# Performance work log

Measured on AMD Instinct MI355X. Metric: run time of the kernel, lower is better.

The kernel has to match this reference:

```python
import jax, jax.numpy as jnp
import numpy as np

EMBED_DIM = 1024
NUM_HEADS = 16
HEAD_DIM = EMBED_DIM // NUM_HEADS


def setup_inputs() -> dict:
    key = jax.random.key(0)
    k1, k2, k3 = jax.random.split(key, 3)
    B, S = 2, 2048
    x = jax.random.normal(k1, (B, S, EMBED_DIM), dtype=jnp.float32)
    # Xavier-uniform-style init for dense kernels
    lim_qkv = float(np.sqrt(6.0 / (EMBED_DIM + 3 * EMBED_DIM)))
    w_qkv = jax.random.uniform(k2, (EMBED_DIM, 3 * EMBED_DIM), jnp.float32, -lim_qkv, lim_qkv)
    b_qkv = jnp.zeros((3 * EMBED_DIM,), jnp.float32)
    lim_out = float(np.sqrt(6.0 / (EMBED_DIM + EMBED_DIM)))
    w_out = jax.random.uniform(k3, (EMBED_DIM, EMBED_DIM), jnp.float32, -lim_out, lim_out)
    b_out = jnp.zeros((EMBED_DIM,), jnp.float32)
    return {"x": x, "w_qkv": w_qkv, "b_qkv": b_qkv, "w_out": w_out, "b_out": b_out}


def reference(x, w_qkv, b_qkv, w_out, b_out):
    B, S, E = x.shape
    qkv = x @ w_qkv + b_qkv                       # [B, S, 3E]
    qkv = qkv.reshape(B, S, NUM_HEADS, 3 * HEAD_DIM)
    qkv = qkv.transpose(0, 2, 1, 3)               # [B, H, S, 3*dh]
    q, k, v = jnp.split(qkv, 3, axis=-1)          # each [B, H, S, dh]
    scale = 1.0 / jnp.sqrt(jnp.asarray(HEAD_DIM, x.dtype))
    logits = jnp.einsum('bhqd,bhkd->bhqk', q, k) * scale  # [B, H, S, S]
    attn = jax.nn.softmax(logits, axis=-1)
    vals = jnp.einsum('bhqk,bhkd->bhqd', attn, v)  # [B, H, S, dh]
    vals = vals.transpose(0, 2, 1, 3).reshape(B, S, E)
    return vals @ w_out + b_out
```

## Files before the change

kernel.cpp:

```cpp
#include <hip/hip_runtime.h>
#include <cstdint>

typedef unsigned short u16;
typedef unsigned int u32;
typedef __attribute__((ext_vector_type(8))) short bf16x8;
typedef __attribute__((ext_vector_type(4))) float f32x4;

#if __has_builtin(__builtin_amdgcn_exp2f)
#define EXP2(x) __builtin_amdgcn_exp2f(x)
#else
#define EXP2(x) exp2f(x)
#endif

__device__ __forceinline__ u16 f2bf(float f) {
  unsigned u = __float_as_uint(f);
  u += 0x7fffu + ((u >> 16) & 1u);
  return (u16)(u >> 16);
}
__device__ __forceinline__ u32 pk_bf16(float lo, float hi) {
#if __has_builtin(__builtin_amdgcn_cvt_pk_bf16_f32)
  auto r = __builtin_amdgcn_cvt_pk_bf16_f32(lo, hi);
  return __builtin_bit_cast(u32, r);
#else
  u32 a = __float_as_uint(lo), b = __float_as_uint(hi);
  a += 0x7fffu + ((a >> 16) & 1u);
  b += 0x7fffu + ((b >> 16) & 1u);
  return (a >> 16) | (b & 0xffff0000u);
#endif
}

__device__ __forceinline__ void async_load16(const void* g, void* l) {
  typedef const __attribute__((address_space(1))) void* gp_t;
  typedef __attribute__((address_space(3))) void* lp_t;
  __builtin_amdgcn_global_load_lds((gp_t)(uintptr_t)g, (lp_t)(uintptr_t)l, 16, 0, 0);
}

__global__ __launch_bounds__(256) void cvt_f32_bf16(
    const float* __restrict__ src, u16* __restrict__ dst)
{
  const size_t i = ((size_t)blockIdx.x * 256 + threadIdx.x) * 8;
  const float4 a = *(const float4*)(src + i);
  const float4 b = *(const float4*)(src + i + 4);
  union { u16 u[8]; bf16x8 v; } p;
  p.u[0] = f2bf(a.x); p.u[1] = f2bf(a.y); p.u[2] = f2bf(a.z); p.u[3] = f2bf(a.w);
  p.u[4] = f2bf(b.x); p.u[5] = f2bf(b.y); p.u[6] = f2bf(b.z); p.u[7] = f2bf(b.w);
  *(bf16x8*)(dst + i) = p.v;
}

__global__ __launch_bounds__(256) void transpose_cvt2(
    const float* __restrict__ wqkv, u16* __restrict__ dqkv,
    const float* __restrict__ wout, u16* __restrict__ dout)
{
  __shared__ u16 tile[64][65];
  const int t = threadIdx.x;
  const int r = t >> 2, c0 = (t & 3) * 16;
  const bool isOut = blockIdx.x >= 48;
  const float* src = isOut ? wout : wqkv;
  u16* dst = isOut ? dout : dqkv;
  const int cols = isOut ? 1024 : 3072;
  const int rows = 1024;
  const int tc = (isOut ? (blockIdx.x - 48) : blockIdx.x) * 64;
  const int tr = blockIdx.y * 64;
  const float* sp = src + (size_t)(tr + r) * cols + tc + c0;
#pragma unroll
  for (int i = 0; i < 16; i += 4) {
    const float4 v = *(const float4*)(sp + i);
    tile[r][c0 + i + 0] = f2bf(v.x);
    tile[r][c0 + i + 1] = f2bf(v.y);
    tile[r][c0 + i + 2] = f2bf(v.z);
    tile[r][c0 + i + 3] = f2bf(v.w);
  }
  __syncthreads();
  u16* dp = dst + (size_t)(tc + r) * rows + tr + c0;
#pragma unroll
  for (int i = 0; i < 16; ++i) dp[i] = tile[c0 + i][r];
}

__global__ __launch_bounds__(256) void transpose_v(
    const u16* __restrict__ src, u16* __restrict__ dst)
{
  __shared__ u16 tile[64][72];
  const int t = threadIdx.x;
  const int r = t >> 2, c0 = (t & 3) * 16;
  const int bh = blockIdx.y, s0 = blockIdx.x * 64;
  const u16* sp = src + ((size_t)bh * 2048 + s0 + r) * 64 + c0;
  union { u16 u[8]; bf16x8 v; } a, b;
  a.v = *(const bf16x8*)sp;
  b.v = *(const bf16x8*)(sp + 8);
#pragma unroll
  for (int i = 0; i < 8; ++i) tile[r][c0 + i] = a.u[i];
#pragma unroll
  for (int i = 0; i < 8; ++i) tile[r][c0 + 8 + i] = b.u[i];
  __syncthreads();
  union { u16 u[8]; bf16x8 v; } x, y;
#pragma unroll
  for (int i = 0; i < 8; ++i) x.u[i] = tile[c0 + i][r];
#pragma unroll
  for (int i = 0; i < 8; ++i) y.u[i] = tile[c0 + 8 + i][r];
  u16* dp = dst + ((size_t)bh * 64 + r) * 2048 + s0 + c0;
  *(bf16x8*)dp = x.v;
  *(bf16x8*)(dp + 8) = y.v;
}

__global__ __launch_bounds__(256) void gemm_qkv(
    const u16* __restrict__ A, const u16* __restrict__ Bt, const float* __restrict__ bias,
    u16* __restrict__ Qp, u16* __restrict__ Kp, u16* __restrict__ Vp, int Kd)
{
  __shared__ __align__(16) u16 As[128 * 32];
  __shared__ __align__(16) u16 Bs[128 * 32];
  const int t = threadIdx.x;
  const int lane = t & 63, wave = t >> 6;
  const int quad = lane >> 4, m16 = lane & 15;
  const int mb = blockIdx.y * 128, nb = blockIdx.x * 128;
  const int wr = (wave & 1) * 64, wc = (wave >> 1) * 64;

  const int srow = t >> 2;
  const int scol = (t & 3) * 8;
  const u16* Ag0 = A + (size_t)(mb + srow) * Kd + scol;
  const u16* Ag1 = Ag0 + (size_t)64 * Kd;
  const u16* Bg0 = Bt + (size_t)(nb + srow) * Kd + scol;
  const u16* Bg1 = Bg0 + (size_t)64 * Kd;
  u16* AsD = As + t * 8;
  u16* BsD = Bs + t * 8;

  f32x4 acc[4][4] = {};

  for (int k0 = 0; k0 < Kd; k0 += 32) {
    __syncthreads();
    async_load16(Ag0 + k0, AsD);
    async_load16(Ag1 + k0, AsD + 2048);
    async_load16(Bg0 + k0, BsD);
    async_load16(Bg1 + k0, BsD + 2048);
    __syncthreads();
    bf16x8 af[4], bfr[4];
#pragma unroll
    for (int i = 0; i < 4; ++i)
      af[i] = *(const bf16x8*)(As + (wr + i * 16 + m16) * 32 + quad * 8);
#pragma unroll
    for (int i = 0; i < 4; ++i)
      bfr[i] = *(const bf16x8*)(Bs + (wc + i * 16 + m16) * 32 + quad * 8);
#pragma unroll
    for (int i = 0; i < 4; ++i)
#pragma unroll
      for (int j = 0; j < 4; ++j)
        acc[i][j] = __builtin_amdgcn_mfma_f32_16x16x32_bf16(af[i], bfr[j], acc[i][j], 0, 0, 0);
  }

#pragma unroll
  for (int j = 0; j < 4; ++j) {
    const int base = nb + wc + j * 16;
    const float bv = bias[base + m16];
    const int seg = base >> 6;
    const int h = seg / 3;
    const int which = seg - h * 3;
    const int d = (base & 63) + m16;
    const float qs = (which == 0) ? 0.18033688011112042f : 1.0f;
#pragma unroll
    for (int i = 0; i < 4; ++i)
#pragma unroll
      for (int r = 0; r < 4; ++r) {
        const int row = mb + wr + i * 16 + quad * 4 + r;
        const int b = row >> 11, sI = row & 2047;
        const u16 v = f2bf((acc[i][j][r] + bv) * qs);
        const size_t idx = (((size_t)((b << 4) | h)) * 2048 + sI) * 64 + d;
        if (which == 0)      Qp[idx] = v;
        else if (which == 1) Kp[idx] = v;
        else                 Vp[idx] = v;
      }
  }
}

__global__ __launch_bounds__(256) void gemm_out(
    const u16* __restrict__ A, const u16* __restrict__ Bt, const float* __restrict__ bias,
    float* __restrict__ Outp)
{
  const int Kd = 1024;
  __shared__ __align__(16) u16 As[64 * 32];
  __shared__ __align__(16) u16 Bs[128 * 32];
  const int t = threadIdx.x;
  const int lane = t & 63, wave = t >> 6;
  const int quad = lane >> 4, m16 = lane & 15;
  const int mb = blockIdx.y * 64, nb = blockIdx.x * 128;
  const int wr = (wave & 1) * 32, wc = (wave >> 1) * 64;

  const int srow = t >> 2;
  const int scol = (t & 3) * 8;
  const u16* Ag0 = A + (size_t)(mb + srow) * Kd + scol;
  const u16* Bg0 = Bt + (size_t)(nb + srow) * Kd + scol;
  const u16* Bg1 = Bg0 + (size_t)64 * Kd;
  u16* AsD = As + t * 8;
  u16* BsD = Bs + t * 8;

  f32x4 acc[2][4] = {};

  for (int k0 = 0; k0 < Kd; k0 += 32) {
    __syncthreads();
    async_load16(Ag0 + k0, AsD);
    async_load16(Bg0 + k0, BsD);
    async_load16(Bg1 + k0, BsD + 2048);
    __syncthreads();
    bf16x8 af[2], bfr[4];
#pragma unroll
    for (int i = 0; i < 2; ++i)
      af[i] = *(const bf16x8*)(As + (wr + i * 16 + m16) * 32 + quad * 8);
#pragma unroll
    for (int j = 0; j < 4; ++j)
      bfr[j] = *(const bf16x8*)(Bs + (wc + j * 16 + m16) * 32 + quad * 8);
#pragma unroll
    for (int i = 0; i < 2; ++i)
#pragma unroll
      for (int j = 0; j < 4; ++j)
        acc[i][j] = __builtin_amdgcn_mfma_f32_16x16x32_bf16(af[i], bfr[j], acc[i][j], 0, 0, 0);
  }

#pragma unroll
  for (int j = 0; j < 4; ++j) {
    const int col = nb + wc + j * 16 + m16;
    const float bv = bias[col];
#pragma unroll
    for (int i = 0; i < 2; ++i)
#pragma unroll
      for (int r = 0; r < 4; ++r) {
        const int row = mb + wr + i * 16 + quad * 4 + r;
        Outp[(size_t)row * 1024 + col] = acc[i][j][r] + bv;
      }
  }
}

__global__ __launch_bounds__(256) void flash_attn(
    const u16* __restrict__ Q, const u16* __restrict__ K, const u16* __restrict__ Vt,
    u16* __restrict__ O)
{
  const int S = 2048;
  __shared__ __align__(16) u16 Kl[2][64 * 64];
  __shared__ __align__(16) u16 Vl[2][64 * 64];
  __shared__ __align__(16) u32 Pl[4][2][16 * 32];
  const int t = threadIdx.x;
  const int lane = t & 63, w = t >> 6;
  const int quad = lane >> 4, m16 = lane & 15;

  const int f = blockIdx.x;
  const int wi = f >> 3;
  const int bh = (f & 7) + 8 * (wi & 3);
  const int q0 = (wi >> 2) * 128;

  const u16* Qb = Q + (size_t)bh * S * 64;
  const u16* Kb = K + (size_t)bh * S * 64;
  const u16* Vb = Vt + (size_t)bh * 64 * S;

  bf16x8 qf[2][2];
#pragma unroll
  for (int g = 0; g < 2; ++g)
#pragma unroll
    for (int ks = 0; ks < 2; ++ks)
      qf[g][ks] = *(const bf16x8*)(Qb + (size_t)(q0 + w * 32 + g * 16 + m16) * 64 + ks * 32 + quad * 8);

  const u16* Kg[2]; const u16* Vg[2]; int soff[2];
#pragma unroll
  for (int l = 0; l < 2; ++l) {
    const int idx = l * 256 + t;
    const int row = idx >> 3, slot = idx & 7;
    const int sg = slot ^ (row & 7);
    Kg[l] = Kb + row * 64 + sg * 8;
    Vg[l] = Vb + (size_t)row * S + sg * 8;
    soff[l] = idx * 8;
  }

  f32x4 ot[2][4] = {};
  f32x4 lr4[2] = {{0.f,0.f,0.f,0.f},{0.f,0.f,0.f,0.f}};
  u32* const Pw0 = &Pl[w][0][0];
  u32* const Pw1 = &Pl[w][1][0];

#define PREFETCH(kvp, B)                                                     \
  do {                                                                       \
    _Pragma("unroll")                                                        \
    for (int l = 0; l < 2; ++l) async_load16(Kg[l] + (kvp) * 64, &Kl[B][soff[l]]); \
    _Pragma("unroll")                                                        \
    for (int l = 0; l < 2; ++l) async_load16(Vg[l] + (kvp), &Vl[B][soff[l]]);      \
  } while (0)

#define STEP(B)                                                              \
  do {                                                                       \
    f32x4 st[2][4] = {};                                                     \
    _Pragma("unroll")                                                        \
    for (int nt = 0; nt < 4; ++nt) {                                         \
      const int j = nt * 16 + m16;                                           \
      const u16* rowp = &Kl[B][j * 64];                                      \
      const bf16x8 kb0 = *(const bf16x8*)(rowp + ((quad ^ (j & 7)) * 8));    \
      const bf16x8 kb1 = *(const bf16x8*)(rowp + (((4 + quad) ^ (j & 7)) * 8)); \
      st[0][nt] = __builtin_amdgcn_mfma_f32_16x16x32_bf16(kb0, qf[0][0], st[0][nt], 0, 0, 0); \
      st[1][nt] = __builtin_amdgcn_mfma_f32_16x16x32_bf16(kb0, qf[1][0], st[1][nt], 0, 0, 0); \
      st[0][nt] = __builtin_amdgcn_mfma_f32_16x16x32_bf16(kb1, qf[0][1], st[0][nt], 0, 0, 0); \
      st[1][nt] = __builtin_amdgcn_mfma_f32_16x16x32_bf16(kb1, qf[1][1], st[1][nt], 0, 0, 0); \
    }                                                                        \
    _Pragma("unroll")                                                        \
    for (int g = 0; g < 2; ++g) {                                            \
      u32* const Pw = g ? Pw1 : Pw0;                                         \
      _Pragma("unroll")                                                      \
      for (int nt = 0; nt < 4; ++nt) {                                       \
        f32x4 p;                                                             \
        _Pragma("unroll")                                                    \
        for (int r = 0; r < 4; ++r) p[r] = EXP2(st[g][nt][r]);               \
        lr4[g] += p;                                                         \
        const u32 lo = pk_bf16(p[0], p[1]);                                  \
        const u32 hi = pk_bf16(p[2], p[3]);                                  \
        const int gp = (2 * nt + (quad >> 1)) ^ (m16 & 7);                   \
        u32* dst = Pw + m16 * 32 + gp * 4 + (quad & 1) * 2;                  \
        *(uint2*)dst = make_uint2(lo, hi);                                   \
      }                                                                      \
    }                                                                        \
    _Pragma("unroll")                                                        \
    for (int ks = 0; ks < 2; ++ks) {                                         \
      const int pg = (ks * 4 + quad) ^ (m16 & 7);                            \
      const bf16x8 pb0 = *(const bf16x8*)(Pw0 + m16 * 32 + pg * 4);          \
      const bf16x8 pb1 = *(const bf16x8*)(Pw1 + m16 * 32 + pg * 4);          \
      _Pragma("unroll")                                                      \
      for (int dt = 0; dt < 4; ++dt) {                                       \
        const int d = dt * 16 + m16;                                         \
        const bf16x8 va = *(const bf16x8*)(&Vl[B][d * 64] + (((ks * 4 + quad) ^ (d & 7)) * 8)); \
        ot[0][dt] = __builtin_amdgcn_mfma_f32_16x16x32_bf16(va, pb0, ot[0][dt], 0, 0, 0); \
        ot[1][dt] = __builtin_amdgcn_mfma_f32_16x16x32_bf16(va, pb1, ot[1][dt], 0, 0, 0); \
      }                                                                      \
    }                                                                        \
  } while (0)

  PREFETCH(0, 0);
  __syncthreads();

  for (int kv0 = 0; kv0 < S; kv0 += 128) {
    PREFETCH(kv0 + 64, 1);
    STEP(0);
    __syncthreads();
    if (kv0 + 128 < S) PREFETCH(kv0 + 128, 0);
    STEP(1);
    __syncthreads();
  }
#undef PREFETCH
#undef STEP

  const int b = bh >> 4, h = bh & 15;
#pragma unroll
  for (int g = 0; g < 2; ++g) {
    float l = lr4[g][0] + lr4[g][1] + lr4[g][2] + lr4[g][3];
    l += __shfl_xor(l, 16, 64);
    l += __shfl_xor(l, 32, 64);
    const float inv = 1.0f / l;
    const int q = q0 + w * 32 + g * 16 + m16;
    u16* base = O + ((size_t)b * 2048 + q) * 1024 + h * 64;
#pragma unroll
    for (int dt = 0; dt < 4; ++dt) {
      const u32 lo = pk_bf16(ot[g][dt][0] * inv, ot[g][dt][1] * inv);
      const u32 hi = pk_bf16(ot[g][dt][2] * inv, ot[g][dt][3] * inv);
      *(uint2*)(base + dt * 16 + quad * 4) = make_uint2(lo, hi);
    }
  }
}

extern "C" void kernel_launch(void* const* d_in, const int* in_sizes, int n_in,
                              void* d_out, int out_size, void* d_ws, size_t ws_size,
                              hipStream_t stream)
{
  const float* x     = (const float*)d_in[0];
  const float* w_qkv = (const float*)d_in[1];
  const float* b_qkv = (const float*)d_in[2];
  const float* w_out = (const float*)d_in[3];
  const float* b_out = (const float*)d_in[4];
  float* out = (float*)d_out;

  u16* ws     = (u16*)d_ws;
  u16* xb     = ws;
  u16* WtQKV  = xb + 4194304;
  u16* WtOut  = WtQKV + 3145728;
  u16* Qm     = WtOut + 1048576;
  u16* Km     = Qm + 4194304;
  u16* Vtm    = Km + 4194304;
  u16* AO     = Vtm + 4194304;
  u16* Vm     = AO;

  cvt_f32_bf16<<<2048, 256, 0, stream>>>(x, xb);
  transpose_cvt2<<<dim3(64, 16), 256, 0, stream>>>(w_qkv, WtQKV, w_out, WtOut);
  gemm_qkv<<<dim3(24, 32), 256, 0, stream>>>(xb, WtQKV, b_qkv, Qm, Km, Vm, 1024);
  transpose_v<<<dim3(32, 32), 256, 0, stream>>>(Vm, Vtm);
  flash_attn<<<512, 256, 0, stream>>>(Qm, Km, Vtm, AO);
  gemm_out<<<dim3(8, 64), 256, 0, stream>>>(AO, WtOut, b_out, out);
}
```

Measured before the change: 202.7 us.

## Stage GEMM epilogues through swizzled LDS for vectorized stores; merge preprocessing kernels

The QKV and output GEMM epilogues now write accumulators into an XOR-swizzled shared-memory tile and then issue 16-byte row-contiguous global stores, replacing scattered 2-byte and 4-byte per-element stores. The x conversion and weight transpose kernels are merged into one launch with block-index dispatch. This targets uncoalesced epilogue writes and one kernel launch, at the cost of more LDS per block (32KB extra), which may lower occupancy, plus an added barrier.

```diff
diff --git a/kernel.cpp b/kernel.cpp
--- a/kernel.cpp
+++ b/kernel.cpp
@@ -35,32 +35,34 @@
   __builtin_amdgcn_global_load_lds((gp_t)(uintptr_t)g, (lp_t)(uintptr_t)l, 16, 0, 0);
 }
 
-__global__ __launch_bounds__(256) void cvt_f32_bf16(
-    const float* __restrict__ src, u16* __restrict__ dst)
-{
-  const size_t i = ((size_t)blockIdx.x * 256 + threadIdx.x) * 8;
-  const float4 a = *(const float4*)(src + i);
-  const float4 b = *(const float4*)(src + i + 4);
-  union { u16 u[8]; bf16x8 v; } p;
-  p.u[0] = f2bf(a.x); p.u[1] = f2bf(a.y); p.u[2] = f2bf(a.z); p.u[3] = f2bf(a.w);
-  p.u[4] = f2bf(b.x); p.u[5] = f2bf(b.y); p.u[6] = f2bf(b.z); p.u[7] = f2bf(b.w);
-  *(bf16x8*)(dst + i) = p.v;
-}
-
-__global__ __launch_bounds__(256) void transpose_cvt2(
+__global__ __launch_bounds__(256) void preprocess(
+    const float* __restrict__ x, u16* __restrict__ xb,
     const float* __restrict__ wqkv, u16* __restrict__ dqkv,
     const float* __restrict__ wout, u16* __restrict__ dout)
 {
   __shared__ u16 tile[64][65];
   const int t = threadIdx.x;
-  const int r = t >> 2, c0 = (t & 3) * 16;
-  const bool isOut = blockIdx.x >= 48;
+  const int bx = blockIdx.x;
+  if (bx < 2048) {
+    const size_t i = ((size_t)bx * 256 + t) * 8;
+    const float4 a = *(const float4*)(x + i);
+    const float4 b = *(const float4*)(x + i + 4);
+    union { u16 u[8]; bf16x8 v; } p;
+    p.u[0] = f2bf(a.x); p.u[1] = f2bf(a.y); p.u[2] = f2bf(a.z); p.u[3] = f2bf(a.w);
+    p.u[4] = f2bf(b.x); p.u[5] = f2bf(b.y); p.u[6] = f2bf(b.z); p.u[7] = f2bf(b.w);
+    *(bf16x8*)(xb + i) = p.v;
+    return;
+  }
+  const int tb = bx - 2048;
+  const int bxx = tb & 63, byy = tb >> 6;
+  const bool isOut = bxx >= 48;
   const float* src = isOut ? wout : wqkv;
   u16* dst = isOut ? dout : dqkv;
   const int cols = isOut ? 1024 : 3072;
   const int rows = 1024;
-  const int tc = (isOut ? (blockIdx.x - 48) : blockIdx.x) * 64;
-  const int tr = blockIdx.y * 64;
+  const int tc = (isOut ? (bxx - 48) : bxx) * 64;
+  const int tr = byy * 64;
+  const int r = t >> 2, c0 = (t & 3) * 16;
   const float* sp = src + (size_t)(tr + r) * cols + tc + c0;
 #pragma unroll
   for (int i = 0; i < 16; i += 4) {
@@ -108,6 +110,7 @@
 {
   __shared__ __align__(16) u16 As[128 * 32];
   __shared__ __align__(16) u16 Bs[128 * 32];
+  __shared__ __align__(16) u16 Cs[128 * 128];
   const int t = threadIdx.x;
   const int lane = t & 63, wave = t >> 6;
   const int quad = lane >> 4, m16 = lane & 15;
@@ -148,25 +151,38 @@
 
 #pragma unroll
   for (int j = 0; j < 4; ++j) {
-    const int base = nb + wc + j * 16;
-    const float bv = bias[base + m16];
-    const int seg = base >> 6;
-    const int h = seg / 3;
-    const int which = seg - h * 3;
-    const int d = (base & 63) + m16;
+    const int col = wc + j * 16 + m16;
+    const int gseg = (nb + col) >> 6;
+    const int h = gseg / 3;
+    const int which = gseg - 3 * h;
+    const float bv = bias[nb + col];
     const float qs = (which == 0) ? 0.18033688011112042f : 1.0f;
 #pragma unroll
     for (int i = 0; i < 4; ++i)
 #pragma unroll
       for (int r = 0; r < 4; ++r) {
-        const int row = mb + wr + i * 16 + quad * 4 + r;
-        const int b = row >> 11, sI = row & 2047;
-        const u16 v = f2bf((acc[i][j][r] + bv) * qs);
-        const size_t idx = (((size_t)((b << 4) | h)) * 2048 + sI) * 64 + d;
-        if (which == 0)      Qp[idx] = v;
-        else if (which == 1) Kp[idx] = v;
-        else                 Vp[idx] = v;
+        const int row = wr + i * 16 + quad * 4 + r;
+        const int sc = ((((col >> 3) ^ (row & 7)) << 3) | (col & 7));
+        Cs[row * 128 + sc] = f2bf((acc[i][j][r] + bv) * qs);
       }
+  }
+  __syncthreads();
+
+  {
+    const int row = t & 127, sSeg = t >> 7;
+    const int seg = (nb >> 6) + sSeg;
+    const int h = seg / 3, which = seg - h * 3;
+    const int m = mb + row;
+    const int b = m >> 11, sI = m & 2047;
+    u16* dstP = (which == 0) ? Qp : (which == 1) ? Kp : Vp;
+    u16* dst = dstP + (((size_t)((b << 4) | h)) * 2048 + sI) * 64;
+    const int rx = row & 7;
+#pragma unroll
+    for (int k = 0; k < 8; ++k) {
+      const int g = (sSeg * 8 + k) ^ rx;
+      const bf16x8 v = *(const bf16x8*)(Cs + row * 128 + g * 8);
+      *(bf16x8*)(dst + k * 8) = v;
+    }
   }
 }
 
@@ -177,6 +193,7 @@
   const int Kd = 1024;
   __shared__ __align__(16) u16 As[64 * 32];
   __shared__ __align__(16) u16 Bs[128 * 32];
+  __shared__ __align__(16) float Cf[64 * 128];
   const int t = threadIdx.x;
   const int lane = t & 63, wave = t >> 6;
   const int quad = lane >> 4, m16 = lane & 15;
@@ -215,15 +232,29 @@
 
 #pragma unroll
   for (int j = 0; j < 4; ++j) {
-    const int col = nb + wc + j * 16 + m16;
-    const float bv = bias[col];
+    const int col = wc + j * 16 + m16;
+    const float bv = bias[nb + col];
 #pragma unroll
     for (int i = 0; i < 2; ++i)
 #pragma unroll
       for (int r = 0; r < 4; ++r) {
-        const int row = mb + wr + i * 16 + quad * 4 + r;
-        Outp[(size_t)row * 1024 + col] = acc[i][j][r] + bv;
+        const int row = wr + i * 16 + quad * 4 + r;
+        const int sc = ((((col >> 2) ^ (row & 7)) << 2) | (col & 3));
+        Cf[row * 128 + sc] = acc[i][j][r] + bv;
       }
+  }
+  __syncthreads();
+
+  {
+    const int row = t & 63, chunk = t >> 6;
+    float* dst = Outp + (size_t)(mb + row) * 1024 + nb + chunk * 32;
+    const int rx = row & 7;
+#pragma unroll
+    for (int k = 0; k < 8; ++k) {
+      const int g = (chunk * 8 + k) ^ rx;
+      const float4 v = *(const float4*)(Cf + row * 128 + g * 4);
+      *(float4*)(dst + k * 4) = v;
+    }
   }
 }
 
@@ -377,8 +408,7 @@
   u16* AO     = Vtm + 4194304;
   u16* Vm     = AO;
 
-  cvt_f32_bf16<<<2048, 256, 0, stream>>>(x, xb);
-  transpose_cvt2<<<dim3(64, 16), 256, 0, stream>>>(w_qkv, WtQKV, w_out, WtOut);
+  preprocess<<<3072, 256, 0, stream>>>(x, xb, w_qkv, WtQKV, w_out, WtOut);
   gemm_qkv<<<dim3(24, 32), 256, 0, stream>>>(xb, WtQKV, b_qkv, Qm, Km, Vm, 1024);
   transpose_v<<<dim3(32, 32), 256, 0, stream>>>(Vm, Vtm);
   flash_attn<<<512, 256, 0, stream>>>(Qm, Km, Vtm, AO);
```

New measurement: 206.9 us. 2.1% more time.

## Double-buffer LDS tiles in both GEMMs and merge preprocessing kernels

Applied to the files above, without the earlier changes.

Both projection GEMMs now keep two LDS buffers, so the async global-to-LDS load for the next K slice is issued before the MFMAs on the current slice. This replaces two barriers per K step with one and overlaps memory latency with compute. Separately, the input conversion and the weight transpose/convert are merged into a single launch, saving one kernel launch. The cost is doubled LDS use per block, which may lower occupancy.

```diff
diff --git a/kernel.cpp b/kernel.cpp
--- a/kernel.cpp
+++ b/kernel.cpp
@@ -35,32 +35,34 @@
   __builtin_amdgcn_global_load_lds((gp_t)(uintptr_t)g, (lp_t)(uintptr_t)l, 16, 0, 0);
 }
 
-__global__ __launch_bounds__(256) void cvt_f32_bf16(
-    const float* __restrict__ src, u16* __restrict__ dst)
-{
-  const size_t i = ((size_t)blockIdx.x * 256 + threadIdx.x) * 8;
-  const float4 a = *(const float4*)(src + i);
-  const float4 b = *(const float4*)(src + i + 4);
-  union { u16 u[8]; bf16x8 v; } p;
-  p.u[0] = f2bf(a.x); p.u[1] = f2bf(a.y); p.u[2] = f2bf(a.z); p.u[3] = f2bf(a.w);
-  p.u[4] = f2bf(b.x); p.u[5] = f2bf(b.y); p.u[6] = f2bf(b.z); p.u[7] = f2bf(b.w);
-  *(bf16x8*)(dst + i) = p.v;
-}
-
-__global__ __launch_bounds__(256) void transpose_cvt2(
+__global__ __launch_bounds__(256) void preprocess(
+    const float* __restrict__ x, u16* __restrict__ xb,
     const float* __restrict__ wqkv, u16* __restrict__ dqkv,
     const float* __restrict__ wout, u16* __restrict__ dout)
 {
   __shared__ u16 tile[64][65];
   const int t = threadIdx.x;
-  const int r = t >> 2, c0 = (t & 3) * 16;
-  const bool isOut = blockIdx.x >= 48;
+  const int bx = blockIdx.x;
+  if (bx < 2048) {
+    const size_t i = ((size_t)bx * 256 + t) * 8;
+    const float4 a = *(const float4*)(x + i);
+    const float4 b = *(const float4*)(x + i + 4);
+    union { u16 u[8]; bf16x8 v; } p;
+    p.u[0] = f2bf(a.x); p.u[1] = f2bf(a.y); p.u[2] = f2bf(a.z); p.u[3] = f2bf(a.w);
+    p.u[4] = f2bf(b.x); p.u[5] = f2bf(b.y); p.u[6] = f2bf(b.z); p.u[7] = f2bf(b.w);
+    *(bf16x8*)(xb + i) = p.v;
+    return;
+  }
+  const int tb = bx - 2048;
+  const int bxx = tb & 63, byy = tb >> 6;
+  const bool isOut = bxx >= 48;
   const float* src = isOut ? wout : wqkv;
   u16* dst = isOut ? dout : dqkv;
   const int cols = isOut ? 1024 : 3072;
   const int rows = 1024;
-  const int tc = (isOut ? (blockIdx.x - 48) : blockIdx.x) * 64;
-  const int tr = blockIdx.y * 64;
+  const int tc = (isOut ? (bxx - 48) : bxx) * 64;
+  const int tr = byy * 64;
+  const int r = t >> 2, c0 = (t & 3) * 16;
   const float* sp = src + (size_t)(tr + r) * cols + tc + c0;
 #pragma unroll
   for (int i = 0; i < 16; i += 4) {
@@ -104,10 +106,11 @@
 
 __global__ __launch_bounds__(256) void gemm_qkv(
     const u16* __restrict__ A, const u16* __restrict__ Bt, const float* __restrict__ bias,
-    u16* __restrict__ Qp, u16* __restrict__ Kp, u16* __restrict__ Vp, int Kd)
-{
-  __shared__ __align__(16) u16 As[128 * 32];
-  __shared__ __align__(16) u16 Bs[128 * 32];
+    u16* __restrict__ Qp, u16* __restrict__ Kp, u16* __restrict__ Vp)
+{
+  const int Kd = 1024;
+  __shared__ __align__(16) u16 As[2][128 * 32];
+  __shared__ __align__(16) u16 Bs[2][128 * 32];
   const int t = threadIdx.x;
   const int lane = t & 63, wave = t >> 6;
   const int quad = lane >> 4, m16 = lane & 15;
@@ -120,31 +123,46 @@
   const u16* Ag1 = Ag0 + (size_t)64 * Kd;
   const u16* Bg0 = Bt + (size_t)(nb + srow) * Kd + scol;
   const u16* Bg1 = Bg0 + (size_t)64 * Kd;
-  u16* AsD = As + t * 8;
-  u16* BsD = Bs + t * 8;
+  const int aoff = t * 8;
 
   f32x4 acc[4][4] = {};
 
-  for (int k0 = 0; k0 < Kd; k0 += 32) {
-    __syncthreads();
-    async_load16(Ag0 + k0, AsD);
-    async_load16(Ag1 + k0, AsD + 2048);
-    async_load16(Bg0 + k0, BsD);
-    async_load16(Bg1 + k0, BsD + 2048);
-    __syncthreads();
-    bf16x8 af[4], bfr[4];
-#pragma unroll
-    for (int i = 0; i < 4; ++i)
-      af[i] = *(const bf16x8*)(As + (wr + i * 16 + m16) * 32 + quad * 8);
-#pragma unroll
-    for (int i = 0; i < 4; ++i)
-      bfr[i] = *(const bf16x8*)(Bs + (wc + i * 16 + m16) * 32 + quad * 8);
-#pragma unroll
-    for (int i = 0; i < 4; ++i)
-#pragma unroll
-      for (int j = 0; j < 4; ++j)
-        acc[i][j] = __builtin_amdgcn_mfma_f32_16x16x32_bf16(af[i], bfr[j], acc[i][j], 0, 0, 0);
-  }
+#define GPRE(k0, B)                                                          \
+  do {                                                                       \
+    async_load16(Ag0 + (k0), &As[B][aoff]);                                  \
+    async_load16(Ag1 + (k0), &As[B][aoff + 2048]);                           \
+    async_load16(Bg0 + (k0), &Bs[B][aoff]);                                  \
+    async_load16(Bg1 + (k0), &Bs[B][aoff + 2048]);                           \
+  } while (0)
+
+#define GSTEP(B)                                                             \
+  do {                                                                       \
+    bf16x8 af[4], bfr[4];                                                    \
+    _Pragma("unroll")                                                        \
+    for (int i = 0; i < 4; ++i)                                              \
+      af[i] = *(const bf16x8*)(&As[B][(wr + i * 16 + m16) * 32 + quad * 8]); \
+    _Pragma("unroll")                                                        \
+    for (int i = 0; i < 4; ++i)                                              \
+      bfr[i] = *(const bf16x8*)(&Bs[B][(wc + i * 16 + m16) * 32 + quad * 8]); \
+    _Pragma("unroll")                                                        \
+    for (int i = 0; i < 4; ++i)                                              \
+      _Pragma("unroll")                                                      \
+      for (int j = 0; j < 4; ++j)                                            \
+        acc[i][j] = __builtin_amdgcn_mfma_f32_16x16x32_bf16(af[i], bfr[j], acc[i][j], 0, 0, 0); \
+  } while (0)
+
+  GPRE(0, 0);
+  __syncthreads();
+  for (int k0 = 0; k0 < Kd; k0 += 64) {
+    GPRE(k0 + 32, 1);
+    GSTEP(0);
+    __syncthreads();
+    if (k0 + 64 < Kd) GPRE(k0 + 64, 0);
+    GSTEP(1);
+    __syncthreads();
+  }
+#undef GPRE
+#undef GSTEP
 
 #pragma unroll
   for (int j = 0; j < 4; ++j) {
@@ -175,8 +193,8 @@
     float* __restrict__ Outp)
 {
   const int Kd = 1024;
-  __shared__ __align__(16) u16 As[64 * 32];
-  __shared__ __align__(16) u16 Bs[128 * 32];
+  __shared__ __align__(16) u16 As[2][64 * 32];
+  __shared__ __align__(16) u16 Bs[2][128 * 32];
   const int t = threadIdx.x;
   const int lane = t & 63, wave = t >> 6;
   const int quad = lane >> 4, m16 = lane & 15;
@@ -188,30 +206,45 @@
   const u16* Ag0 = A + (size_t)(mb + srow) * Kd + scol;
   const u16* Bg0 = Bt + (size_t)(nb + srow) * Kd + scol;
   const u16* Bg1 = Bg0 + (size_t)64 * Kd;
-  u16* AsD = As + t * 8;
-  u16* BsD = Bs + t * 8;
+  const int aoff = t * 8;
 
   f32x4 acc[2][4] = {};
 
-  for (int k0 = 0; k0 < Kd; k0 += 32) {
-    __syncthreads();
-    async_load16(Ag0 + k0, AsD);
-    async_load16(Bg0 + k0, BsD);
-    async_load16(Bg1 + k0, BsD + 2048);
-    __syncthreads();
-    bf16x8 af[2], bfr[4];
-#pragma unroll
-    for (int i = 0; i < 2; ++i)
-      af[i] = *(const bf16x8*)(As + (wr + i * 16 + m16) * 32 + quad * 8);
-#pragma unroll
-    for (int j = 0; j < 4; ++j)
-      bfr[j] = *(const bf16x8*)(Bs + (wc + j * 16 + m16) * 32 + quad * 8);
-#pragma unroll
-    for (int i = 0; i < 2; ++i)
-#pragma unroll
-      for (int j = 0; j < 4; ++j)
-        acc[i][j] = __builtin_amdgcn_mfma_f32_16x16x32_bf16(af[i], bfr[j], acc[i][j], 0, 0, 0);
-  }
+#define OPRE(k0, B)                                                          \
+  do {                                                                       \
+    async_load16(Ag0 + (k0), &As[B][aoff]);                                  \
+    async_load16(Bg0 + (k0), &Bs[B][aoff]);                                  \
+    async_load16(Bg1 + (k0), &Bs[B][aoff + 2048]);                           \
+  } while (0)
+
+#define OSTEP(B)                                                             \
+  do {                                                                       \
+    bf16x8 af[2], bfr[4];                                                    \
+    _Pragma("unroll")                                                        \
+    for (int i = 0; i < 2; ++i)                                              \
+      af[i] = *(const bf16x8*)(&As[B][(wr + i * 16 + m16) * 32 + quad * 8]); \
+    _Pragma("unroll")                                                        \
+    for (int j = 0; j < 4; ++j)                                              \
+      bfr[j] = *(const bf16x8*)(&Bs[B][(wc + j * 16 + m16) * 32 + quad * 8]); \
+    _Pragma("unroll")                                                        \
+    for (int i = 0; i < 2; ++i)                                              \
+      _Pragma("unroll")                                                      \
+      for (int j = 0; j < 4; ++j)                                            \
+        acc[i][j] = __builtin_amdgcn_mfma_f32_16x16x32_bf16(af[i], bfr[j], acc[i][j], 0, 0, 0); \
+  } while (0)
+
+  OPRE(0, 0);
+  __syncthreads();
+  for (int k0 = 0; k0 < Kd; k0 += 64) {
+    OPRE(k0 + 32, 1);
+    OSTEP(0);
+    __syncthreads();
+    if (k0 + 64 < Kd) OPRE(k0 + 64, 0);
+    OSTEP(1);
+    __syncthreads();
+  }
+#undef OPRE
+#undef OSTEP
 
 #pragma unroll
   for (int j = 0; j < 4; ++j) {
@@ -377,9 +410,8 @@
   u16* AO     = Vtm + 4194304;
   u16* Vm     = AO;
 
-  cvt_f32_bf16<<<2048, 256, 0, stream>>>(x, xb);
-  transpose_cvt2<<<dim3(64, 16), 256, 0, stream>>>(w_qkv, WtQKV, w_out, WtOut);
-  gemm_qkv<<<dim3(24, 32), 256, 0, stream>>>(xb, WtQKV, b_qkv, Qm, Km, Vm, 1024);
+  preprocess<<<3072, 256, 0, stream>>>(x, xb, w_qkv, WtQKV, w_out, WtOut);
+  gemm_qkv<<<dim3(24, 32), 256, 0, stream>>>(xb, WtQKV, b_qkv, Qm, Km, Vm);
   transpose_v<<<dim3(32, 32), 256, 0, stream>>>(Vm, Vtm);
   flash_attn<<<512, 256, 0, stream>>>(Qm, Km, Vtm, AO);
   gemm_out<<<dim3(8, 64), 256, 0, stream>>>(AO, WtOut, b_out, out);
```

Measured after the change: 193.7 us. 4.4% less time.
